# Kernel tuning notes

Measured on AMD Instinct MI355X. Metric: run time of the kernel, lower is better.

Reference implementation:

```python
import jax, jax.numpy as jnp
import numpy as np


def setup_inputs() -> dict:
    key = jax.random.key(0)
    ks = jax.random.split(key, 6)
    B, S, DK = 4, 2048, 1024
    scale = 1.0 / np.sqrt(DK)  # keep weight magnitudes sane like torch init
    return {
        "q": jax.random.normal(ks[0], (B, S, DK), jnp.float32),
        "k": jax.random.normal(ks[1], (B, S, DK), jnp.float32),
        "v": jax.random.normal(ks[2], (B, S, DK), jnp.float32),
        "wq": jax.random.normal(ks[3], (DK, DK), jnp.float32) * scale,
        "wk": jax.random.normal(ks[4], (DK, DK), jnp.float32) * scale,
        "wv": jax.random.normal(ks[5], (DK, DK), jnp.float32) * scale,
    }


def reference(q, k, v, wq, wk, wv):
    dk = q.shape[-1]
    # nn.Linear: y = x @ W^T  (weights stored [out, in])
    qp = jnp.einsum("bsd,ed->bse", q, wq)
    kp = jnp.einsum("bsd,ed->bse", k, wk)
    vp = jnp.einsum("bsd,ed->bse", v, wv)
    norm = 1.0 / jnp.sqrt(jnp.asarray(dk, qp.dtype))
    s = jnp.einsum("bqd,bkd->bqk", qp, kp) * norm  # [B, S, S]
    # module computes exp(s)/sum(exp(s)) manually; mathematically softmax
    e = jnp.exp(s)
    attention = e / jnp.sum(e, axis=-1, keepdims=True)
    # dropout is identity in eval mode (deterministic reference)
    return jnp.einsum("bqk,bkd->bqd", attention, vp)
```

## Files before the change

kernel.cpp:

```cpp
#include <hip/hip_runtime.h>

typedef _Float16 f16;
typedef _Float16 f16x4 __attribute__((ext_vector_type(4)));
typedef _Float16 f16x8 __attribute__((ext_vector_type(8)));
typedef float    fx4   __attribute__((ext_vector_type(4)));

#define MODE_PROJ   0
#define MODE_SCORES 1
#define MODE_PV     2

constexpr int Bsz = 4;
constexpr int S   = 2048;
constexpr int DK  = 1024;
constexpr int BM = 128, BN = 128, BK = 32;
constexpr long SD   = (long)S * DK;
constexpr long SS   = (long)S * S;
constexpr long BIGN = (long)Bsz * S * DK;

__device__ __forceinline__ void glds16(const f16* g, f16* l) {
    __builtin_amdgcn_global_load_lds(
        (const __attribute__((address_space(1))) void*)g,
        (__attribute__((address_space(3))) void*)l, 16, 0, 0);
}

__global__ __launch_bounds__(256)
void convert_kernel(const float* q, const float* k, const float* v,
                    const float* wq, const float* wk, const float* wv)
{
    int bx = blockIdx.x;
    const float* src;
    int blk;
    if (bx < 12288) {
        int t = bx >> 12; blk = bx & 4095;
        src = (t == 0) ? q : (t == 1) ? k : v;
    } else {
        int u = bx - 12288;
        int t = u >> 9; blk = u & 511;
        src = (t == 0) ? wq : (t == 1) ? wk : wv;
    }
    size_t off = (size_t)blk * 2048 + (size_t)threadIdx.x * 8;
    float4 f0 = *(const float4*)(src + off);
    float4 f1 = *(const float4*)(src + off + 4);
    __syncthreads();
    f16x8 h = {(f16)f0.x, (f16)f0.y, (f16)f0.z, (f16)f0.w,
               (f16)f1.x, (f16)f1.y, (f16)f1.z, (f16)f1.w};
    *(f16x8*)((char*)src + (size_t)blk * 8192 + (size_t)threadIdx.x * 16) = h;
}

__device__ __forceinline__ size_t pp(int r, int c) {
    return ((size_t)(r >> 1) << 12) + ((r & 1) << 10) + c;
}

template<int MODE>
__global__ __launch_bounds__(256, 4)
void gemm_kernel(const f16* A0, const f16* A1, const f16* A2,
                 const f16* B0, const f16* B1, const f16* B2,
                 void* O0, void* O1, float* rowsum,
                 int lda, int ldb, int K, int ldo)
{
    __shared__ f16 lA[BM * BK];
    __shared__ f16 lB[BN * BK];

    const int tid = threadIdx.x;
    const int z   = blockIdx.z;
    const int row0 = blockIdx.y * BM;
    const int col0 = blockIdx.x * BN;
    const int lane = tid & 63;
    const int quad = lane >> 4;
    const int cn   = lane & 15;
    const int w    = tid >> 6;
    const int wm   = w >> 1;
    const int wn   = w & 1;

    const f16 *Ap, *Bp;
    if constexpr (MODE == MODE_PROJ) {
        Ap = (z == 0) ? A0 : (z == 1) ? A1 : A2;
        Bp = (z == 0) ? B0 : (z == 1) ? B1 : B2;
    } else if constexpr (MODE == MODE_SCORES) {
        Ap = A0 + (long)z * SD;  Bp = B0 + (long)z * SD;
        rowsum += (long)z * S;
    } else {
        Ap = A0 + (long)z * SS;  Bp = B0 + (long)z * SD;
        rowsum += (long)z * S;
    }

    fx4 acc[4][4];
    #pragma unroll
    for (int mt = 0; mt < 4; ++mt)
        #pragma unroll
        for (int nt = 0; nt < 4; ++nt)
            acc[mt][nt] = (fx4){0.f, 0.f, 0.f, 0.f};

    const int lr = lane >> 2;
    const int lc = (lane & 3) * 8;

    for (int k0 = 0; k0 < K; k0 += BK) {
        __syncthreads();
        #pragma unroll
        for (int i = 0; i < 2; ++i) {
            int rb = w * 32 + i * 16;
            if constexpr (MODE == MODE_PROJ) {
                int ra  = row0 + rb + lr;
                int rbt = col0 + rb + lr;
                glds16(Ap + pp(ra,  k0 + lc), &lA[rb * BK]);
                glds16(Bp + pp(rbt, k0 + lc), &lB[rb * BK]);
            } else {
                glds16(Ap + (size_t)(row0 + rb + lr) * lda + k0 + lc, &lA[rb * BK]);
                glds16(Bp + (size_t)(col0 + rb + lr) * ldb + k0 + lc, &lB[rb * BK]);
            }
        }
        __syncthreads();

        f16x8 af[4], bf[4];
        #pragma unroll
        for (int mt = 0; mt < 4; ++mt)
            af[mt] = *(const f16x8*)&lA[(wm * 64 + mt * 16 + cn) * BK + quad * 8];
        #pragma unroll
        for (int nt = 0; nt < 4; ++nt)
            bf[nt] = *(const f16x8*)&lB[(wn * 64 + nt * 16 + cn) * BK + quad * 8];
        #pragma unroll
        for (int mt = 0; mt < 4; ++mt)
            #pragma unroll
            for (int nt = 0; nt < 4; ++nt)
                acc[mt][nt] = __builtin_amdgcn_mfma_f32_16x16x32_f16(
                    af[mt], bf[nt], acc[mt][nt], 0, 0, 0);
    }

    if constexpr (MODE == MODE_PROJ) {
        if (z < 2) {
            f16* O = (f16*)O0 + (long)z * BIGN;
            #pragma unroll
            for (int mt = 0; mt < 4; ++mt) {
                int r0 = row0 + wm * 64 + mt * 16 + quad * 4;
                #pragma unroll
                for (int nt = 0; nt < 4; ++nt) {
                    int c = col0 + wn * 64 + nt * 16 + cn;
                    #pragma unroll
                    for (int reg = 0; reg < 4; ++reg)
                        O[(size_t)(r0 + reg) * DK + c] = (f16)acc[mt][nt][reg];
                }
            }
        } else {
            #pragma unroll
            for (int mt = 0; mt < 4; ++mt) {
                int r0 = row0 + wm * 64 + mt * 16 + quad * 4;
                int b  = r0 >> 11;
                int s  = r0 & 2047;
                f16* O = (f16*)O1 + (long)b * SD;
                #pragma unroll
                for (int nt = 0; nt < 4; ++nt) {
                    int c = col0 + wn * 64 + nt * 16 + cn;
                    f16x4 h = {(f16)acc[mt][nt][0], (f16)acc[mt][nt][1],
                               (f16)acc[mt][nt][2], (f16)acc[mt][nt][3]};
                    *(f16x4*)&O[(size_t)c * S + s] = h;
                }
            }
        }
    } else if constexpr (MODE == MODE_SCORES) {
        f16* O = (f16*)O0 + (long)z * SS;
        const float scale = 0.03125f;
        float rs[4][4];
        #pragma unroll
        for (int mt = 0; mt < 4; ++mt)
            #pragma unroll
            for (int reg = 0; reg < 4; ++reg) rs[mt][reg] = 0.f;
        #pragma unroll
        for (int mt = 0; mt < 4; ++mt) {
            int r0 = row0 + wm * 64 + mt * 16 + quad * 4;
            #pragma unroll
            for (int nt = 0; nt < 4; ++nt) {
                int c = col0 + wn * 64 + nt * 16 + cn;
                #pragma unroll
                for (int reg = 0; reg < 4; ++reg) {
                    float vv = __expf(acc[mt][nt][reg] * scale);
                    rs[mt][reg] += vv;
                    O[(size_t)(r0 + reg) * ldo + c] = (f16)vv;
                }
            }
        }
        #pragma unroll
        for (int mt = 0; mt < 4; ++mt) {
            int r0 = row0 + wm * 64 + mt * 16 + quad * 4;
            #pragma unroll
            for (int reg = 0; reg < 4; ++reg) {
                float vv = rs[mt][reg];
                vv += __shfl_xor(vv, 1);
                vv += __shfl_xor(vv, 2);
                vv += __shfl_xor(vv, 4);
                vv += __shfl_xor(vv, 8);
                if (cn == 0) atomicAdd(&rowsum[r0 + reg], vv);
            }
        }
    } else {
        float* O = (float*)O0 + (long)z * SD;
        #pragma unroll
        for (int mt = 0; mt < 4; ++mt) {
            int r0 = row0 + wm * 64 + mt * 16 + quad * 4;
            fx4 rsv = *(const fx4*)&rowsum[r0];
            fx4 inv = {1.f / rsv[0], 1.f / rsv[1], 1.f / rsv[2], 1.f / rsv[3]};
            #pragma unroll
            for (int nt = 0; nt < 4; ++nt) {
                int c = col0 + wn * 64 + nt * 16 + cn;
                #pragma unroll
                for (int reg = 0; reg < 4; ++reg)
                    O[(size_t)(r0 + reg) * ldo + c] = acc[mt][nt][reg] * inv[reg];
            }
        }
    }
}

extern "C" void kernel_launch(void* const* d_in, const int* in_sizes, int n_in,
                              void* d_out, int out_size, void* d_ws, size_t ws_size,
                              hipStream_t stream) {
    const float* q  = (const float*)d_in[0];
    const float* k  = (const float*)d_in[1];
    const float* v  = (const float*)d_in[2];
    const float* wq = (const float*)d_in[3];
    const float* wk = (const float*)d_in[4];
    const float* wv = (const float*)d_in[5];
    float* out = (float*)d_out;

    char* ws = (char*)d_ws;
    f16*   qp     = (f16*)(ws);
    f16*   kp     = (f16*)(ws + ((size_t)16 << 20));
    f16*   vpT    = (f16*)(ws + ((size_t)32 << 20));
    f16*   E      = (f16*)(ws + ((size_t)48 << 20));
    float* rowsum = (float*)(ws + ((size_t)80 << 20));

    hipMemsetAsync(rowsum, 0, (size_t)Bsz * S * sizeof(float), stream);

    convert_kernel<<<13824, 256, 0, stream>>>(q, k, v, wq, wk, wv);

    const f16* qh  = (const f16*)q;
    const f16* kh  = (const f16*)k;
    const f16* vh  = (const f16*)v;
    const f16* wqh = (const f16*)wq;
    const f16* wkh = (const f16*)wk;
    const f16* wvh = (const f16*)wv;

    dim3 blk(256);
    gemm_kernel<MODE_PROJ><<<dim3(DK / BN, (Bsz * S) / BM, 3), blk, 0, stream>>>(
        qh, kh, vh, wqh, wkh, wvh, qp, vpT, nullptr, DK, DK, DK, DK);
    gemm_kernel<MODE_SCORES><<<dim3(S / BN, S / BM, Bsz), blk, 0, stream>>>(
        qp, nullptr, nullptr, kp, nullptr, nullptr, E, nullptr, rowsum,
        DK, DK, DK, S);
    gemm_kernel<MODE_PV><<<dim3(DK / BN, S / BM, Bsz), blk, 0, stream>>>(
        E, nullptr, nullptr, vpT, nullptr, nullptr, out, nullptr, rowsum,
        S, S, S, DK);
}
```

Baseline: 335.0 us.

## Double K-tile depth, XOR-swizzle LDS layout, and remap block indices

Raises the K tile from 32 to 64 so each barrier pair covers twice as many MFMAs. An XOR swizzle on 16-byte chunks is applied to both the global-to-LDS loads and the fragment reads, meant to avoid LDS bank conflicts from the wider row stride. The 3D grid is flattened into a 1D block id with row-major-fastest mapping, so consecutive blocks share the same B column tile for L2 reuse. The exp is also rewritten as exp2 with a prescaled log2e; doubling LDS per block may reduce occupancy.

```diff
diff --git a/kernel.cpp b/kernel.cpp
--- a/kernel.cpp
+++ b/kernel.cpp
@@ -12,7 +12,7 @@
 constexpr int Bsz = 4;
 constexpr int S   = 2048;
 constexpr int DK  = 1024;
-constexpr int BM = 128, BN = 128, BK = 32;
+constexpr int BM = 128, BN = 128, BK = 64;
 constexpr long SD   = (long)S * DK;
 constexpr long SS   = (long)S * S;
 constexpr long BIGN = (long)Bsz * S * DK;
@@ -62,9 +62,12 @@
     __shared__ f16 lB[BN * BK];
 
     const int tid = threadIdx.x;
-    const int z   = blockIdx.z;
-    const int row0 = blockIdx.y * BM;
-    const int col0 = blockIdx.x * BN;
+    const int id  = blockIdx.x;
+    const int z   = blockIdx.y;
+    int row0, col0;
+    if constexpr (MODE == MODE_PROJ) { row0 = (id & 63) * BM; col0 = (id >> 6) * BN; }
+    else                             { row0 = (id & 15) * BM; col0 = (id >> 4) * BN; }
+
     const int lane = tid & 63;
     const int quad = lane >> 4;
     const int cn   = lane & 15;
@@ -91,39 +94,47 @@
         for (int nt = 0; nt < 4; ++nt)
             acc[mt][nt] = (fx4){0.f, 0.f, 0.f, 0.f};
 
-    const int lr = lane >> 2;
-    const int lc = (lane & 3) * 8;
+    const int lr8 = lane >> 3;
+    const int swc = (lane & 7) ^ lr8;
+    const int lcS = swc << 3;
 
     for (int k0 = 0; k0 < K; k0 += BK) {
         __syncthreads();
         #pragma unroll
-        for (int i = 0; i < 2; ++i) {
-            int rb = w * 32 + i * 16;
+        for (int i = 0; i < 4; ++i) {
+            int rb = w * 32 + i * 8;
             if constexpr (MODE == MODE_PROJ) {
-                int ra  = row0 + rb + lr;
-                int rbt = col0 + rb + lr;
-                glds16(Ap + pp(ra,  k0 + lc), &lA[rb * BK]);
-                glds16(Bp + pp(rbt, k0 + lc), &lB[rb * BK]);
+                glds16(Ap + pp(row0 + rb + lr8, k0 + lcS), &lA[rb * BK]);
+                glds16(Bp + pp(col0 + rb + lr8, k0 + lcS), &lB[rb * BK]);
             } else {
-                glds16(Ap + (size_t)(row0 + rb + lr) * lda + k0 + lc, &lA[rb * BK]);
-                glds16(Bp + (size_t)(col0 + rb + lr) * ldb + k0 + lc, &lB[rb * BK]);
+                glds16(Ap + (size_t)(row0 + rb + lr8) * lda + k0 + lcS, &lA[rb * BK]);
+                glds16(Bp + (size_t)(col0 + rb + lr8) * ldb + k0 + lcS, &lB[rb * BK]);
             }
         }
         __syncthreads();
 
-        f16x8 af[4], bf[4];
-        #pragma unroll
-        for (int mt = 0; mt < 4; ++mt)
-            af[mt] = *(const f16x8*)&lA[(wm * 64 + mt * 16 + cn) * BK + quad * 8];
-        #pragma unroll
-        for (int nt = 0; nt < 4; ++nt)
-            bf[nt] = *(const f16x8*)&lB[(wn * 64 + nt * 16 + cn) * BK + quad * 8];
-        #pragma unroll
-        for (int mt = 0; mt < 4; ++mt)
-            #pragma unroll
-            for (int nt = 0; nt < 4; ++nt)
-                acc[mt][nt] = __builtin_amdgcn_mfma_f32_16x16x32_f16(
-                    af[mt], bf[nt], acc[mt][nt], 0, 0, 0);
+        #pragma unroll
+        for (int kh = 0; kh < 2; ++kh) {
+            f16x8 af[4], bf[4];
+            #pragma unroll
+            for (int mt = 0; mt < 4; ++mt) {
+                int r = wm * 64 + mt * 16 + cn;
+                int ch = ((kh << 2) | quad) ^ (r & 7);
+                af[mt] = *(const f16x8*)&lA[r * BK + ch * 8];
+            }
+            #pragma unroll
+            for (int nt = 0; nt < 4; ++nt) {
+                int r = wn * 64 + nt * 16 + cn;
+                int ch = ((kh << 2) | quad) ^ (r & 7);
+                bf[nt] = *(const f16x8*)&lB[r * BK + ch * 8];
+            }
+            #pragma unroll
+            for (int mt = 0; mt < 4; ++mt)
+                #pragma unroll
+                for (int nt = 0; nt < 4; ++nt)
+                    acc[mt][nt] = __builtin_amdgcn_mfma_f32_16x16x32_f16(
+                        af[mt], bf[nt], acc[mt][nt], 0, 0, 0);
+        }
     }
 
     if constexpr (MODE == MODE_PROJ) {
@@ -158,7 +169,7 @@
         }
     } else if constexpr (MODE == MODE_SCORES) {
         f16* O = (f16*)O0 + (long)z * SS;
-        const float scale = 0.03125f;
+        const float sl2e = 0.03125f * 1.44269504f;
         float rs[4][4];
         #pragma unroll
         for (int mt = 0; mt < 4; ++mt)
@@ -172,7 +183,7 @@
                 int c = col0 + wn * 64 + nt * 16 + cn;
                 #pragma unroll
                 for (int reg = 0; reg < 4; ++reg) {
-                    float vv = __expf(acc[mt][nt][reg] * scale);
+                    float vv = exp2f(acc[mt][nt][reg] * sl2e);
                     rs[mt][reg] += vv;
                     O[(size_t)(r0 + reg) * ldo + c] = (f16)vv;
                 }
@@ -239,12 +250,12 @@
     const f16* wvh = (const f16*)wv;
 
     dim3 blk(256);
-    gemm_kernel<MODE_PROJ><<<dim3(DK / BN, (Bsz * S) / BM, 3), blk, 0, stream>>>(
+    gemm_kernel<MODE_PROJ><<<dim3(512, 3), blk, 0, stream>>>(
         qh, kh, vh, wqh, wkh, wvh, qp, vpT, nullptr, DK, DK, DK, DK);
-    gemm_kernel<MODE_SCORES><<<dim3(S / BN, S / BM, Bsz), blk, 0, stream>>>(
+    gemm_kernel<MODE_SCORES><<<dim3(256, 4), blk, 0, stream>>>(
         qp, nullptr, nullptr, kp, nullptr, nullptr, E, nullptr, rowsum,
         DK, DK, DK, S);
-    gemm_kernel<MODE_PV><<<dim3(DK / BN, S / BM, Bsz), blk, 0, stream>>>(
+    gemm_kernel<MODE_PV><<<dim3(128, 4), blk, 0, stream>>>(
         E, nullptr, nullptr, vpT, nullptr, nullptr, out, nullptr, rowsum,
         S, S, S, DK);
 }
```

Measured after the change: 298.8 us. -10.8%, faster.
